# Optimization experiments

Hardware: AMD Instinct MI355X
Metric: run time of the kernel (lower is better)

The kernel has to match this reference:

```python
import jax, jax.numpy as jnp
import numpy as np

NEG_INF = -1e12
ALPHA = 0.01  # LeakyReLU slope


def setup_inputs() -> dict:
    key = jax.random.key(0)
    ks = jax.random.split(key, 12)
    K, N, DIN, H1, DOUT, FC1 = 64, 1024, 16, 4, 8, 54
    X = jax.random.normal(ks[0], (K, N, DIN), dtype=jnp.float32)
    adj = jax.random.randint(ks[1], (N, N), 0, 2, dtype=jnp.int32)
    # Xavier-uniform-ish init scale (gain 1.414)
    def xavier(k, shape):
        fan_in, fan_out = shape[0], shape[-1]
        lim = 1.414 * np.sqrt(6.0 / (fan_in + fan_out))
        return jax.random.uniform(k, shape, jnp.float32, -lim, lim)
    W1 = xavier(ks[2], (DIN, H1))
    a1 = xavier(ks[3], (2 * H1, 1))
    W2 = xavier(ks[4], (H1, DOUT))
    a2 = xavier(ks[5], (2 * DOUT, 1))
    fc1_w = xavier(ks[6], (N * DOUT, FC1))
    fc1_b = jnp.zeros((FC1,), jnp.float32)
    out_w = xavier(ks[7], (FC1, N))
    out_b = jnp.zeros((N,), jnp.float32)
    return {"X": X, "adj": adj, "W1": W1, "a1": a1, "W2": W2, "a2": a2,
            "fc1_w": fc1_w, "fc1_b": fc1_b, "out_w": out_w, "out_b": out_b}


def _gat_layer(h_in, adj, W, a):
    # h: [K, N, F]
    h = jnp.matmul(h_in, W)
    Fdim = W.shape[1]
    # concat(h_i, h_j) @ a  ==  (h_i . a[:F]) + (h_j . a[F:])
    f1 = jnp.matmul(h, a[:Fdim, 0])  # [K, N]
    f2 = jnp.matmul(h, a[Fdim:, 0])  # [K, N]
    e = jax.nn.leaky_relu(f1[:, :, None] + f2[:, None, :], ALPHA)  # [K, N, N]
    e = jnp.where(adj[None, :, :] > 0, e, NEG_INF)
    att = jax.nn.softmax(e, axis=2)
    return jnp.einsum('kij,kjf->kif', att, h)


def reference(X, adj, W1, a1, W2, a2, fc1_w, fc1_b, out_w, out_b):
    x = jax.nn.relu(_gat_layer(X, adj, W1, a1))
    x = jax.nn.relu(_gat_layer(x, adj, W2, a2))
    x = x.reshape(x.shape[0], -1)  # [K, N*dim_output]
    x = jax.nn.relu(jnp.matmul(x, fc1_w) + fc1_b)
    return jnp.matmul(x, out_w) + out_b  # [K, N] q-values
```

## Files before the change

kernel.cpp:

```cpp
#include <hip/hip_runtime.h>
#include <hip/hip_bf16.h>

constexpr int K    = 64;
constexpr int N    = 1024;
constexpr int DIN  = 16;
constexpr int H1   = 4;
constexpr int DOUT = 8;
constexpr int FC1  = 54;

#define ALPHA_F   (0.01f)
#define LOG2E_F   (1.4426950408889634f)

typedef unsigned int uint;
typedef short  bf16x8 __attribute__((ext_vector_type(8)));
typedef float  f32x4  __attribute__((ext_vector_type(4)));

__device__ inline float fast_exp2(float x) {
#if __has_builtin(__builtin_amdgcn_exp2f)
    return __builtin_amdgcn_exp2f(x);
#else
    return __expf(x * 0.6931471805599453f);
#endif
}

__device__ inline uint pk_bf16(float a, float b) {
    union { __hip_bfloat162 h; uint u; } v;
    v.h = __float22bfloat162_rn(make_float2(a, b));
    return v.u;
}


__global__ __launch_bounds__(512) void prep_kernel(
        const int* __restrict__ adj, unsigned long long* __restrict__ maskM,
        const float* __restrict__ X, const float* __restrict__ W1,
        const float* __restrict__ a1,
        uint4* __restrict__ HB1, float* __restrict__ f11, float* __restrict__ f21,
        float* __restrict__ y) {
    int b = blockIdx.x;
    if (b < 512) {
        int wv = threadIdx.x >> 6, lane = threadIdx.x & 63;
        int g = b * 8 + wv;
        #pragma unroll
        for (int uu = 0; uu < 4; uu++) {
            int u = g * 4 + uu;
            int jw = u >> 10;
            int i  = u & 1023;
            int v = adj[i * N + (jw << 6) + lane];
            unsigned long long m = __ballot(v > 0);
            if (lane == 0) maskM[i * 16 + jw] = m;
        }
    } else if (b < 640) {
        __shared__ float hrow[512 * 4];
        const int bb  = b - 512;
        const int k   = bb >> 1;
        const int j0  = (bb & 1) * 512;
        const int tid = threadIdx.x;
        const int idx = k * N + j0 + tid;
        const float4* x4 = (const float4*)(X + (size_t)idx * DIN);
        float hv_[H1] = {0.f, 0.f, 0.f, 0.f};
        #pragma unroll
        for (int q = 0; q < 4; q++) {
            float4 xv = x4[q];
            #pragma unroll
            for (int f = 0; f < H1; f++) {
                hv_[f] += xv.x * W1[(q * 4 + 0) * H1 + f] + xv.y * W1[(q * 4 + 1) * H1 + f]
                        + xv.z * W1[(q * 4 + 2) * H1 + f] + xv.w * W1[(q * 4 + 3) * H1 + f];
            }
        }
        float s1 = 0.f, s2 = 0.f;
        #pragma unroll
        for (int f = 0; f < H1; f++) { s1 += hv_[f] * a1[f]; s2 += hv_[f] * a1[H1 + f]; }
        f11[idx] = s1 * LOG2E_F;
        f21[idx] = s2 * LOG2E_F;
        #pragma unroll
        for (int f = 0; f < H1; f++) hrow[tid * 4 + f] = hv_[f];
        __syncthreads();
        uint4* HBk = HB1 + (size_t)k * 2048 + (j0 >> 5) * 64;
        #pragma unroll
        for (int e = tid; e < 1024; e += 512) {
            int cl = e >> 6, l = e & 63, q = (l >> 4), n = l & 15;
            uint4 dw;
            if (n < H1) {
                const float* hp = hrow + (cl * 32 + q * 8) * 4 + n;
                dw.x = pk_bf16(hp[0],  hp[4]);
                dw.y = pk_bf16(hp[8],  hp[12]);
                dw.z = pk_bf16(hp[16], hp[20]);
                dw.w = pk_bf16(hp[24], hp[28]);
            } else if (n == H1) {
                dw = make_uint4(0x3f803f80u, 0x3f803f80u, 0x3f803f80u, 0x3f803f80u);
            } else {
                dw = make_uint4(0u, 0u, 0u, 0u);
            }
            HBk[cl * 64 + l] = dw;
        }
    } else {
        for (int t = threadIdx.x; t < 4096; t += 512) y[t] = 0.f;
    }
}

template <int F, bool FUSE>
__global__ __launch_bounds__(512, 4) void gat_attn_mfma(
        const unsigned long long* __restrict__ maskM,
        const uint4* __restrict__ HBin,
        const float* __restrict__ f1,
        const float* __restrict__ f2,
        const float* __restrict__ W2,
        const float* __restrict__ a2,
        const float* __restrict__ fc1w,
        uint4* __restrict__ HBout,
        float* __restrict__ y,
        float* __restrict__ o_f1,
        float* __restrict__ o_f2) {
    __shared__ float F2s[1024];
    __shared__ float XPa[8][16][5];
    __shared__ float XPb[8][16][9];
    __shared__ float YPs[8][64];

    const int tid  = threadIdx.x;
    const int lane = tid & 63;
    const int wv   = tid >> 6;
    const int quad = lane >> 4;
    const int n16  = lane & 15;
    const int k    = blockIdx.x >> 3;

    if (tid < 256)
        ((float4*)F2s)[tid] = ((const float4*)(f2 + k * N))[tid];
    __syncthreads();

    const int itile = (blockIdx.x & 7) * 8 + wv;
    const int ibase = itile * 16;
    const int irow  = ibase + n16;
    const float f1v = f1[k * N + irow];
    const uint4* mrow = (const uint4*)((const char*)maskM + (size_t)irow * 128);
    const uint4* HBk  = HBin + (size_t)k * 2048;

    f32x4 acc = {0.f, 0.f, 0.f, 0.f};
    union { bf16x8 v; uint u[4]; } af;
    union { bf16x8 v; uint4 q; }  bfrag;

    #pragma unroll 2
    for (int g = 0; g < 8; g++) {
        const uint4 Mg = mrow[g];
        #pragma unroll
        for (int cc = 0; cc < 4; cc++) {
            const int c = g * 4 + cc;
            const uint mdw = (cc == 0) ? Mg.x : (cc == 1) ? Mg.y
                           : (cc == 2) ? Mg.z : Mg.w;
            const uint mb  = (mdw >> (quad * 8)) & 0xffu;
            float4 fa = *(const float4*)(F2s + c * 32 + quad * 8);
            float4 fb = *(const float4*)(F2s + c * 32 + quad * 8 + 4);
            bfrag.q = HBk[c * 64 + lane];
            float f2e[8] = {fa.x, fa.y, fa.z, fa.w, fb.x, fb.y, fb.z, fb.w};
            float pv[8];
            #pragma unroll
            for (int jj = 0; jj < 8; jj++) {
                float x = f1v + f2e[jj];
                float e = fmaxf(x, ALPHA_F * x);
                float p = fast_exp2(e);
                pv[jj] = (mb & (1u << jj)) ? p : 0.f;
            }
            #pragma unroll
            for (int pr = 0; pr < 4; pr++)
                af.u[pr] = pk_bf16(pv[2 * pr], pv[2 * pr + 1]);
            acc = __builtin_amdgcn_mfma_f32_16x16x32_bf16(af.v, bfrag.v, acc, 0, 0, 0);
        }
    }

    #pragma unroll
    for (int r = 0; r < 4; r++) {
        float den = __shfl(acc[r], (lane & 48) + F);
        float inv = (den > 0.f) ? 1.f / den : 0.f;
        float xo  = fmaxf(acc[r] * inv, 0.f);
        int m = quad * 4 + r;
        if constexpr (FUSE) {
            if (n16 < F) XPa[wv][m][n16] = xo;
        } else {
            if (n16 < F) XPb[wv][m][n16] = xo;
        }
    }

    if constexpr (FUSE) {
        __syncthreads();
        if (lane < 16) {
            const int m = lane;
            float x0 = XPa[wv][m][0], x1 = XPa[wv][m][1];
            float x2v = XPa[wv][m][2], x3 = XPa[wv][m][3];
            float hv[DOUT];
            #pragma unroll
            for (int f = 0; f < DOUT; f++) {
                hv[f] = x0 * W2[f]      + x1 * W2[8 + f]
                      + x2v * W2[16 + f] + x3 * W2[24 + f];
            }
            float t1 = 0.f, t2 = 0.f;
            #pragma unroll
            for (int f = 0; f < DOUT; f++) { t1 += hv[f] * a2[f]; t2 += hv[f] * a2[DOUT + f]; }
            const int row = k * N + ibase + m;
            o_f1[row] = t1 * LOG2E_F;
            o_f2[row] = t2 * LOG2E_F;
            #pragma unroll
            for (int f = 0; f < DOUT; f++) XPb[wv][m][f] = hv[f];
        }
        __syncthreads();
        if (lane < 32) {
            const int c2    = ibase >> 5;
            const int qhalf = (ibase >> 4) & 1;
            const int ql    = lane >> 4;
            const int n     = lane & 15;
            const int q     = qhalf * 2 + ql;
            uint4 dw;
            if (n < DOUT) {
                dw.x = pk_bf16(XPb[wv][ql * 8 + 0][n], XPb[wv][ql * 8 + 1][n]);
                dw.y = pk_bf16(XPb[wv][ql * 8 + 2][n], XPb[wv][ql * 8 + 3][n]);
                dw.z = pk_bf16(XPb[wv][ql * 8 + 4][n], XPb[wv][ql * 8 + 5][n]);
                dw.w = pk_bf16(XPb[wv][ql * 8 + 6][n], XPb[wv][ql * 8 + 7][n]);
            } else if (n == DOUT) {
                dw = make_uint4(0x3f803f80u, 0x3f803f80u, 0x3f803f80u, 0x3f803f80u);
            } else {
                dw = make_uint4(0u, 0u, 0u, 0u);
            }
            HBout[(size_t)k * 2048 + c2 * 64 + q * 16 + n] = dw;
        }
    } else {
        const int ceff = (lane < FC1) ? lane : 0;
        const float* wb = fc1w + (size_t)ibase * DOUT * FC1;
        float pacc = 0.f;
        #pragma unroll 8
        for (int mm = 0; mm < 128; mm++) {
            float xv = XPb[wv][mm >> 3][mm & 7];
            pacc = fmaf(xv, wb[(size_t)mm * FC1 + ceff], pacc);
        }
        YPs[wv][lane] = pacc;
        __syncthreads();
        if (tid < 64) {
            float s = 0.f;
            #pragma unroll
            for (int w = 0; w < 8; w++) s += YPs[w][tid];
            if (tid < FC1) atomicAdd(&y[k * FC1 + tid], s);
        }
    }
}

__global__ __launch_bounds__(512) void fc2_kernel(
        const float* __restrict__ y, const float* __restrict__ fc1b,
        const float* __restrict__ outw, const float* __restrict__ outb,
        float* __restrict__ out) {
    __shared__ float ybuf[FC1];
    const int t = threadIdx.x;
    const int k = blockIdx.y;
    if (t < FC1) ybuf[t] = fmaxf(y[k * FC1 + t] + fc1b[t], 0.f);
    __syncthreads();
    const int n = blockIdx.x * 512 + t;
    float s = outb[n];
    #pragma unroll 6
    for (int cc = 0; cc < FC1; cc++)
        s += ybuf[cc] * outw[(size_t)cc * N + n];
    out[(size_t)k * N + n] = s;
}

extern "C" void kernel_launch(void* const* d_in, const int* in_sizes, int n_in,
                              void* d_out, int out_size, void* d_ws, size_t ws_size,
                              hipStream_t stream) {
    const float* X     = (const float*)d_in[0];
    const int*   adj   = (const int*)  d_in[1];
    const float* W1    = (const float*)d_in[2];
    const float* a1    = (const float*)d_in[3];
    const float* W2    = (const float*)d_in[4];
    const float* a2    = (const float*)d_in[5];
    const float* fc1w  = (const float*)d_in[6];
    const float* fc1b  = (const float*)d_in[7];
    const float* outw  = (const float*)d_in[8];
    const float* outb  = (const float*)d_in[9];
    float* out = (float*)d_out;

    float* ws  = (float*)d_ws;
    float* f11 = ws;
    float* f21 = f11 + 65536;
    float* f12 = f21 + 65536;
    float* f22 = f12 + 65536;
    float* y   = f22 + 65536;
    unsigned long long* mM = (unsigned long long*)(y + 4096);
    uint4* HB1 = (uint4*)(y + 4096 + 32768);
    uint4* HB2 = HB1 + 131072;

    prep_kernel<<<dim3(641), dim3(512), 0, stream>>>(
        adj, mM, X, W1, a1, HB1, f11, f21, y);

    gat_attn_mfma<4, true><<<dim3(K * 8), dim3(512), 0, stream>>>(
        mM, HB1, f11, f21, W2, a2, nullptr, HB2, nullptr, f12, f22);

    gat_attn_mfma<8, false><<<dim3(K * 8), dim3(512), 0, stream>>>(
        mM, HB2, f12, f22, nullptr, nullptr, fc1w, nullptr, y, nullptr, nullptr);

    fc2_kernel<<<dim3(2, K), dim3(512), 0, stream>>>(y, fc1b, outw, outb, out);
}
```

Measured before the change: 124.8 us.

## Split GAT attention j-range across wave pairs and replace atomics with partial sums

Result: no change. 126.6 us (+1.4%).

```diff
diff --git a/kernel.cpp b/kernel.cpp
--- a/kernel.cpp
+++ b/kernel.cpp
@@ -34,8 +34,7 @@
         const int* __restrict__ adj, unsigned long long* __restrict__ maskM,
         const float* __restrict__ X, const float* __restrict__ W1,
         const float* __restrict__ a1,
-        uint4* __restrict__ HB1, float* __restrict__ f11, float* __restrict__ f21,
-        float* __restrict__ y) {
+        uint4* __restrict__ HB1, float* __restrict__ f11, float* __restrict__ f21) {
     int b = blockIdx.x;
     if (b < 512) {
         int wv = threadIdx.x >> 6, lane = threadIdx.x & 63;
@@ -49,7 +48,7 @@
             unsigned long long m = __ballot(v > 0);
             if (lane == 0) maskM[i * 16 + jw] = m;
         }
-    } else if (b < 640) {
+    } else {
         __shared__ float hrow[512 * 4];
         const int bb  = b - 512;
         const int k   = bb >> 1;
@@ -93,13 +92,11 @@
             }
             HBk[cl * 64 + l] = dw;
         }
-    } else {
-        for (int t = threadIdx.x; t < 4096; t += 512) y[t] = 0.f;
     }
 }
 
 template <int F, bool FUSE>
-__global__ __launch_bounds__(512, 4) void gat_attn_mfma(
+__global__ __launch_bounds__(512, 8) void gat_attn_mfma(
         const unsigned long long* __restrict__ maskM,
         const uint4* __restrict__ HBin,
         const float* __restrict__ f1,
@@ -108,26 +105,30 @@
         const float* __restrict__ a2,
         const float* __restrict__ fc1w,
         uint4* __restrict__ HBout,
-        float* __restrict__ y,
+        float* __restrict__ yp,
         float* __restrict__ o_f1,
         float* __restrict__ o_f2) {
     __shared__ float F2s[1024];
-    __shared__ float XPa[8][16][5];
-    __shared__ float XPb[8][16][9];
+    __shared__ float ACC[4][64][4];
+    __shared__ float XPa[4][16][5];
+    __shared__ float XPb[4][16][9];
     __shared__ float YPs[8][64];
 
     const int tid  = threadIdx.x;
     const int lane = tid & 63;
-    const int wv   = tid >> 6;
+    const int w    = tid >> 6;
+    const int wv   = w >> 1;
+    const int half = w & 1;
     const int quad = lane >> 4;
     const int n16  = lane & 15;
-    const int k    = blockIdx.x >> 3;
+    const int k    = blockIdx.x >> 4;
+    const int s4   = blockIdx.x & 15;
 
     if (tid < 256)
         ((float4*)F2s)[tid] = ((const float4*)(f2 + k * N))[tid];
     __syncthreads();
 
-    const int itile = (blockIdx.x & 7) * 8 + wv;
+    const int itile = s4 * 4 + wv;
     const int ibase = itile * 16;
     const int irow  = ibase + n16;
     const float f1v = f1[k * N + irow];
@@ -139,7 +140,8 @@
     union { bf16x8 v; uint4 q; }  bfrag;
 
     #pragma unroll 2
-    for (int g = 0; g < 8; g++) {
+    for (int gg = 0; gg < 4; gg++) {
+        const int g = half * 4 + gg;
         const uint4 Mg = mrow[g];
         #pragma unroll
         for (int cc = 0; cc < 4; cc++) {
@@ -166,22 +168,31 @@
         }
     }
 
-    #pragma unroll
-    for (int r = 0; r < 4; r++) {
-        float den = __shfl(acc[r], (lane & 48) + F);
-        float inv = (den > 0.f) ? 1.f / den : 0.f;
-        float xo  = fmaxf(acc[r] * inv, 0.f);
-        int m = quad * 4 + r;
-        if constexpr (FUSE) {
-            if (n16 < F) XPa[wv][m][n16] = xo;
-        } else {
-            if (n16 < F) XPb[wv][m][n16] = xo;
+    if (half) {
+        #pragma unroll
+        for (int r = 0; r < 4; r++) ACC[wv][lane][r] = acc[r];
+    }
+    __syncthreads();
+    if (!half) {
+        #pragma unroll
+        for (int r = 0; r < 4; r++) acc[r] += ACC[wv][lane][r];
+        #pragma unroll
+        for (int r = 0; r < 4; r++) {
+            float den = __shfl(acc[r], (lane & 48) + F);
+            float inv = (den > 0.f) ? 1.f / den : 0.f;
+            float xo  = fmaxf(acc[r] * inv, 0.f);
+            int m = quad * 4 + r;
+            if constexpr (FUSE) {
+                if (n16 < F) XPa[wv][m][n16] = xo;
+            } else {
+                if (n16 < F) XPb[wv][m][n16] = xo;
+            }
         }
     }
 
     if constexpr (FUSE) {
         __syncthreads();
-        if (lane < 16) {
+        if (!half && lane < 16) {
             const int m = lane;
             float x0 = XPa[wv][m][0], x1 = XPa[wv][m][1];
             float x2v = XPa[wv][m][2], x3 = XPa[wv][m][3];
@@ -201,7 +212,7 @@
             for (int f = 0; f < DOUT; f++) XPb[wv][m][f] = hv[f];
         }
         __syncthreads();
-        if (lane < 32) {
+        if (!half && lane < 32) {
             const int c2    = ibase >> 5;
             const int qhalf = (ibase >> 4) & 1;
             const int ql    = lane >> 4;
@@ -221,33 +232,39 @@
             HBout[(size_t)k * 2048 + c2 * 64 + q * 16 + n] = dw;
         }
     } else {
+        __syncthreads();
         const int ceff = (lane < FC1) ? lane : 0;
-        const float* wb = fc1w + (size_t)ibase * DOUT * FC1;
+        const float* wb = fc1w + ((size_t)ibase * DOUT + half * 64) * FC1;
         float pacc = 0.f;
         #pragma unroll 8
-        for (int mm = 0; mm < 128; mm++) {
-            float xv = XPb[wv][mm >> 3][mm & 7];
+        for (int mm = 0; mm < 64; mm++) {
+            float xv = XPb[wv][half * 8 + (mm >> 3)][mm & 7];
             pacc = fmaf(xv, wb[(size_t)mm * FC1 + ceff], pacc);
         }
-        YPs[wv][lane] = pacc;
+        YPs[w][lane] = pacc;
         __syncthreads();
         if (tid < 64) {
             float s = 0.f;
             #pragma unroll
-            for (int w = 0; w < 8; w++) s += YPs[w][tid];
-            if (tid < FC1) atomicAdd(&y[k * FC1 + tid], s);
+            for (int ww = 0; ww < 8; ww++) s += YPs[ww][tid];
+            yp[blockIdx.x * 64 + tid] = s;
         }
     }
 }
 
 __global__ __launch_bounds__(512) void fc2_kernel(
-        const float* __restrict__ y, const float* __restrict__ fc1b,
+        const float* __restrict__ yp, const float* __restrict__ fc1b,
         const float* __restrict__ outw, const float* __restrict__ outb,
         float* __restrict__ out) {
     __shared__ float ybuf[FC1];
     const int t = threadIdx.x;
     const int k = blockIdx.y;
-    if (t < FC1) ybuf[t] = fmaxf(y[k * FC1 + t] + fc1b[t], 0.f);
+    if (t < FC1) {
+        float s = fc1b[t];
+        #pragma unroll
+        for (int sl = 0; sl < 16; sl++) s += yp[((k << 4) + sl) * 64 + t];
+        ybuf[t] = fmaxf(s, 0.f);
+    }
     __syncthreads();
     const int n = blockIdx.x * 512 + t;
     float s = outb[n];
@@ -277,19 +294,19 @@
     float* f21 = f11 + 65536;
     float* f12 = f21 + 65536;
     float* f22 = f12 + 65536;
-    float* y   = f22 + 65536;
-    unsigned long long* mM = (unsigned long long*)(y + 4096);
-    uint4* HB1 = (uint4*)(y + 4096 + 32768);
+    float* yp  = f22 + 65536;
+    unsigned long long* mM = (unsigned long long*)(yp + 65536);
+    uint4* HB1 = (uint4*)(yp + 65536 + 32768);
     uint4* HB2 = HB1 + 131072;
 
-    prep_kernel<<<dim3(641), dim3(512), 0, stream>>>(
-        adj, mM, X, W1, a1, HB1, f11, f21, y);
-
-    gat_attn_mfma<4, true><<<dim3(K * 8), dim3(512), 0, stream>>>(
+    prep_kernel<<<dim3(640), dim3(512), 0, stream>>>(
+        adj, mM, X, W1, a1, HB1, f11, f21);
+
+    gat_attn_mfma<H1, true><<<dim3(K * 16), dim3(512), 0, stream>>>(
         mM, HB1, f11, f21, W2, a2, nullptr, HB2, nullptr, f12, f22);
 
-    gat_attn_mfma<8, false><<<dim3(K * 8), dim3(512), 0, stream>>>(
-        mM, HB2, f12, f22, nullptr, nullptr, fc1w, nullptr, y, nullptr, nullptr);
-
-    fc2_kernel<<<dim3(2, K), dim3(512), 0, stream>>>(y, fc1b, outw, outb, out);
-}
+    gat_attn_mfma<DOUT, false><<<dim3(K * 16), dim3(512), 0, stream>>>(
+        mM, HB2, f12, f22, nullptr, nullptr, fc1w, nullptr, yp, nullptr, nullptr);
+
+    fc2_kernel<<<dim3(2, K), dim3(512), 0, stream>>>(yp, fc1b, outw, outb, out);
+}
```

## Remap GAT blocks across XCDs and replace atomic FC1 reduction with partials

Applied to the files above, without the earlier changes.

Result: slower. 128.0 us (+2.5%).

```diff
diff --git a/kernel.cpp b/kernel.cpp
--- a/kernel.cpp
+++ b/kernel.cpp
@@ -34,8 +34,7 @@
         const int* __restrict__ adj, unsigned long long* __restrict__ maskM,
         const float* __restrict__ X, const float* __restrict__ W1,
         const float* __restrict__ a1,
-        uint4* __restrict__ HB1, float* __restrict__ f11, float* __restrict__ f21,
-        float* __restrict__ y) {
+        uint4* __restrict__ HB1, float* __restrict__ f11, float* __restrict__ f21) {
     int b = blockIdx.x;
     if (b < 512) {
         int wv = threadIdx.x >> 6, lane = threadIdx.x & 63;
@@ -49,7 +48,7 @@
             unsigned long long m = __ballot(v > 0);
             if (lane == 0) maskM[i * 16 + jw] = m;
         }
-    } else if (b < 640) {
+    } else {
         __shared__ float hrow[512 * 4];
         const int bb  = b - 512;
         const int k   = bb >> 1;
@@ -93,8 +92,6 @@
             }
             HBk[cl * 64 + l] = dw;
         }
-    } else {
-        for (int t = threadIdx.x; t < 4096; t += 512) y[t] = 0.f;
     }
 }
 
@@ -108,7 +105,7 @@
         const float* __restrict__ a2,
         const float* __restrict__ fc1w,
         uint4* __restrict__ HBout,
-        float* __restrict__ y,
+        float* __restrict__ yp,
         float* __restrict__ o_f1,
         float* __restrict__ o_f2) {
     __shared__ float F2s[1024];
@@ -121,13 +118,15 @@
     const int wv   = tid >> 6;
     const int quad = lane >> 4;
     const int n16  = lane & 15;
-    const int k    = blockIdx.x >> 3;
+    const int bid  = blockIdx.x;
+    const int k    = ((bid & 7) << 3) | ((bid >> 3) & 7);
+    const int s    = bid >> 6;
 
     if (tid < 256)
         ((float4*)F2s)[tid] = ((const float4*)(f2 + k * N))[tid];
     __syncthreads();
 
-    const int itile = (blockIdx.x & 7) * 8 + wv;
+    const int itile = s * 8 + wv;
     const int ibase = itile * 16;
     const int irow  = ibase + n16;
     const float f1v = f1[k * N + irow];
@@ -232,22 +231,27 @@
         YPs[wv][lane] = pacc;
         __syncthreads();
         if (tid < 64) {
-            float s = 0.f;
-            #pragma unroll
-            for (int w = 0; w < 8; w++) s += YPs[w][tid];
-            if (tid < FC1) atomicAdd(&y[k * FC1 + tid], s);
+            float sm = 0.f;
+            #pragma unroll
+            for (int w = 0; w < 8; w++) sm += YPs[w][tid];
+            yp[(k * 8 + s) * 64 + tid] = sm;
         }
     }
 }
 
 __global__ __launch_bounds__(512) void fc2_kernel(
-        const float* __restrict__ y, const float* __restrict__ fc1b,
+        const float* __restrict__ yp, const float* __restrict__ fc1b,
         const float* __restrict__ outw, const float* __restrict__ outb,
         float* __restrict__ out) {
     __shared__ float ybuf[FC1];
     const int t = threadIdx.x;
     const int k = blockIdx.y;
-    if (t < FC1) ybuf[t] = fmaxf(y[k * FC1 + t] + fc1b[t], 0.f);
+    if (t < FC1) {
+        float s = fc1b[t];
+        #pragma unroll
+        for (int sl = 0; sl < 8; sl++) s += yp[((k << 3) + sl) * 64 + t];
+        ybuf[t] = fmaxf(s, 0.f);
+    }
     __syncthreads();
     const int n = blockIdx.x * 512 + t;
     float s = outb[n];
@@ -277,19 +281,19 @@
     float* f21 = f11 + 65536;
     float* f12 = f21 + 65536;
     float* f22 = f12 + 65536;
-    float* y   = f22 + 65536;
-    unsigned long long* mM = (unsigned long long*)(y + 4096);
-    uint4* HB1 = (uint4*)(y + 4096 + 32768);
+    float* yp  = f22 + 65536;
+    unsigned long long* mM = (unsigned long long*)(yp + 32768);
+    uint4* HB1 = (uint4*)(yp + 32768 + 32768);
     uint4* HB2 = HB1 + 131072;
 
-    prep_kernel<<<dim3(641), dim3(512), 0, stream>>>(
-        adj, mM, X, W1, a1, HB1, f11, f21, y);
-
-    gat_attn_mfma<4, true><<<dim3(K * 8), dim3(512), 0, stream>>>(
+    prep_kernel<<<dim3(640), dim3(512), 0, stream>>>(
+        adj, mM, X, W1, a1, HB1, f11, f21);
+
+    gat_attn_mfma<H1, true><<<dim3(K * 8), dim3(512), 0, stream>>>(
         mM, HB1, f11, f21, W2, a2, nullptr, HB2, nullptr, f12, f22);
 
-    gat_attn_mfma<8, false><<<dim3(K * 8), dim3(512), 0, stream>>>(
-        mM, HB2, f12, f22, nullptr, nullptr, fc1w, nullptr, y, nullptr, nullptr);
-
-    fc2_kernel<<<dim3(2, K), dim3(512), 0, stream>>>(y, fc1b, outw, outb, out);
-}
+    gat_attn_mfma<DOUT, false><<<dim3(K * 8), dim3(512), 0, stream>>>(
+        mM, HB2, f12, f22, nullptr, nullptr, fc1w, nullptr, yp, nullptr, nullptr);
+
+    fc2_kernel<<<dim3(2, K), dim3(512), 0, stream>>>(yp, fc1b, outw, outb, out);
+}
```
